# Optimization experiments

Hardware: AMD Instinct MI355X
Metric: run time of the kernel (lower is better)

Reference implementation:

```python
import jax, jax.numpy as jnp
import numpy as np

H = 1024      # hidden_size
I = 4096      # intermediate_size
E = 8         # num_experts
TOP_K = 2
LB_COEF = 0.01


def setup_inputs() -> dict:
    key = jax.random.key(0)
    ks = jax.random.split(key, 8)
    s_h = 1.0 / np.sqrt(H)
    s_i = 1.0 / np.sqrt(I)
    return {
        "x": jax.random.normal(ks[0], (2, 2048, H), dtype=jnp.float32),
        "Wr": jax.random.normal(ks[1], (H, E), dtype=jnp.float32) * s_h,
        "br": jnp.zeros((E,), dtype=jnp.float32),
        "W1": jax.random.normal(ks[2], (E, H, I), dtype=jnp.float32) * s_h,
        "b1": jnp.zeros((E, I), dtype=jnp.float32),
        "W2": jax.random.normal(ks[3], (E, I, H), dtype=jnp.float32) * s_i,
        "b2": jnp.zeros((E, H), dtype=jnp.float32),
    }


def _moe_forward(x, Wr, br, W1, b1, W2, b2):
    B, S, Hd = x.shape
    x_flat = x.reshape(-1, Hd)                      # [T, H]
    T = x_flat.shape[0]

    # ---- Router: softmax probs, top-k, renormalize ----
    logits = x_flat @ Wr + br                       # [T, E]
    probs = jax.nn.softmax(logits, axis=-1)         # [T, E]
    topk_w, topk_idx = jax.lax.top_k(probs, TOP_K)  # [T, K]
    topk_w = topk_w / jnp.sum(topk_w, axis=-1, keepdims=True)

    # ---- Load-balance aux loss (switch-style) ----
    onehot = jax.nn.one_hot(topk_idx, E, dtype=x.dtype)   # [T, K, E]
    frac_tokens = onehot.mean(axis=(0, 1))                 # [E]
    frac_probs = probs.mean(axis=0)                        # [E]
    aux_loss = E * jnp.sum(frac_tokens * frac_probs) * LB_COEF

    # combine_weights[t, e] = routing weight of expert e for token t (0 if unselected)
    combine = jnp.sum(topk_w[..., None] * onehot, axis=1)  # [T, E]

    # ---- Experts: dense per-expert FFN, weighted combine ----
    out = jnp.zeros_like(x_flat)
    for e in range(E):
        h = jax.nn.gelu(x_flat @ W1[e] + b1[e])            # [T, I]
        y = h @ W2[e] + b2[e]                              # [T, H]
        out = out + y * combine[:, e:e + 1]
    return out.reshape(B, S, Hd), aux_loss


def reference(x, Wr, br, W1, b1, W2, b2):
    return _moe_forward(x, Wr, br, W1, b1, W2, b2)
```

## Files before the change

kernel.cpp:

```cpp
#include <hip/hip_runtime.h>
#include <hip/hip_bf16.h>

#define HD 1024
#define ID 4096
#define NE 8
#define NT 4096
#define NSLOT (NT*2)

typedef __attribute__((ext_vector_type(4))) float f32x4;
typedef __attribute__((ext_vector_type(8))) short bf16x8;
typedef __attribute__((ext_vector_type(4))) unsigned int u32x4;
typedef __attribute__((ext_vector_type(2))) unsigned int u32x2;
typedef unsigned short u16;

__device__ __forceinline__ u16 f2b(float f) {
  __hip_bfloat16 h = __float2bfloat16(f);
  return __builtin_bit_cast(unsigned short, h);
}
__device__ __forceinline__ unsigned int pack2(float a, float b) {
  return (unsigned int)f2b(a) | ((unsigned int)f2b(b) << 16);
}
__device__ __forceinline__ void gload16(const void* g, void* l) {
  __builtin_amdgcn_global_load_lds(
      (const __attribute__((address_space(1))) unsigned int*)g,
      (__attribute__((address_space(3))) unsigned int*)l, 16, 0, 0);
}
__device__ __forceinline__ float gelu_tanh(float v) {
  float c = v + 0.044715f * v * v * v;
  return 0.5f * v * (1.0f + tanhf(0.7978845608028654f * c));
}

__global__ void k_convert_x(const float* __restrict__ x, u16* __restrict__ xb) {
  int i = blockIdx.x * 256 + threadIdx.x;
  const f32x4* x4 = (const f32x4*)x;
  f32x4 a = x4[2 * i], b = x4[2 * i + 1];
  u32x4 r;
  r[0] = pack2(a[0], a[1]); r[1] = pack2(a[2], a[3]);
  r[2] = pack2(b[0], b[1]); r[3] = pack2(b[2], b[3]);
  ((u32x4*)xb)[i] = r;
}

__global__ __launch_bounds__(256) void k_transpose_bf16(
    const float* __restrict__ src, u16* __restrict__ dst, int R, int C) {
  __shared__ float tile[64][65];
  int e = blockIdx.z;
  int c0 = blockIdx.x * 64;
  int r0 = blockIdx.y * 64;
  int t = threadIdx.x;
  const float* s = src + (size_t)e * R * C;
#pragma unroll
  for (int i = 0; i < 16; ++i) {
    int r = i * 4 + (t >> 6);
    tile[r][t & 63] = s[(size_t)(r0 + r) * C + c0 + (t & 63)];
  }
  __syncthreads();
  u16* d = dst + (size_t)e * R * C;
#pragma unroll
  for (int i = 0; i < 4; ++i) {
    int c = i * 16 + (t >> 4);
    int rb = (t & 15) * 4;
    u32x2 p;
    p[0] = pack2(tile[rb + 0][c], tile[rb + 1][c]);
    p[1] = pack2(tile[rb + 2][c], tile[rb + 3][c]);
    *(u32x2*)&d[(size_t)(c0 + c) * R + r0 + rb] = p;
  }
}

__global__ __launch_bounds__(256) void k_router(
    const float* __restrict__ x, const float* __restrict__ Wr,
    const float* __restrict__ br, int* __restrict__ cnt,
    int* __restrict__ slotE, int* __restrict__ slotLoc,
    float* __restrict__ slotW, float* __restrict__ probsAll) {
  __shared__ float wrt[NE * HD];
  int t = threadIdx.x;
  for (int i = t; i < NE * HD; i += 256) wrt[(i & 7) * HD + (i >> 3)] = Wr[i];
  __syncthreads();
  int wave = t >> 6, lane = t & 63;
  int token = blockIdx.x * 4 + wave;
  const float* xr = x + (size_t)token * HD;
  float acc[NE] = {0, 0, 0, 0, 0, 0, 0, 0};
#pragma unroll 4
  for (int j = 0; j < 16; ++j) {
    int h = j * 64 + lane;
    float xv = xr[h];
#pragma unroll
    for (int e = 0; e < NE; ++e) acc[e] += xv * wrt[e * HD + h];
  }
#pragma unroll
  for (int d = 1; d < 64; d <<= 1) {
#pragma unroll
    for (int e = 0; e < NE; ++e) acc[e] += __shfl_xor(acc[e], d, 64);
  }
  if (lane == 0) {
    float lg[NE], p[NE];
    float m = -1e30f;
#pragma unroll
    for (int e = 0; e < NE; ++e) { lg[e] = acc[e] + br[e]; m = fmaxf(m, lg[e]); }
    float s = 0.f;
#pragma unroll
    for (int e = 0; e < NE; ++e) { p[e] = expf(lg[e] - m); s += p[e]; }
    float inv = 1.0f / s;
    int i1 = 0, i2 = -1;
    float v1 = -1.f, v2 = -1.f;
#pragma unroll
    for (int e = 0; e < NE; ++e) {
      p[e] *= inv;
      probsAll[token * NE + e] = p[e];
      if (p[e] > v1) { v2 = v1; i2 = i1; v1 = p[e]; i1 = e; }
      else if (p[e] > v2) { v2 = p[e]; i2 = e; }
    }
    float wsum = v1 + v2;
    int l1 = atomicAdd(&cnt[i1], 1);
    int l2 = atomicAdd(&cnt[i2], 1);
    slotE[token * 2] = i1;     slotLoc[token * 2] = l1;     slotW[token * 2] = v1 / wsum;
    slotE[token * 2 + 1] = i2; slotLoc[token * 2 + 1] = l2; slotW[token * 2 + 1] = v2 / wsum;
  }
}

__global__ __launch_bounds__(256) void k_finalize(
    const float* __restrict__ probsAll, const int* __restrict__ cnt,
    int* __restrict__ off, float* __restrict__ out_aux) {
  __shared__ float red[256];
  int t = threadIdx.x;
  float loc[NE] = {0, 0, 0, 0, 0, 0, 0, 0};
  for (int i = t; i < NT; i += 256) {
#pragma unroll
    for (int e = 0; e < NE; ++e) loc[e] += probsAll[i * NE + e];
  }
  __shared__ float psum[NE];
  for (int e = 0; e < NE; ++e) {
    red[t] = loc[e];
    __syncthreads();
    for (int s = 128; s > 0; s >>= 1) {
      if (t < s) red[t] += red[t + s];
      __syncthreads();
    }
    if (t == 0) psum[e] = red[0];
    __syncthreads();
  }
  if (t == 0) {
    int o = 0;
    float a = 0.f;
    for (int e = 0; e < NE; ++e) {
      off[e] = o;
      o += cnt[e];
      a += ((float)cnt[e] / (float)NSLOT) * (psum[e] / (float)NT);
    }
    off[NE] = o;
    out_aux[0] = (float)NE * a * 0.01f;
  }
}

__global__ void k_scatter(const int* __restrict__ slotE, const int* __restrict__ slotLoc,
                          const float* __restrict__ slotW, const int* __restrict__ off,
                          int* __restrict__ rowTok, float* __restrict__ rowW) {
  int i = blockIdx.x * 256 + threadIdx.x;
  int pos = off[slotE[i]] + slotLoc[i];
  if (pos < 0) pos = 0;
  if (pos >= NSLOT) pos = NSLOT - 1;
  rowTok[pos] = i >> 1;
  rowW[pos] = slotW[i];
}

__global__ __launch_bounds__(256, 2) void k_gemm1(
    const u16* __restrict__ xb, const u16* __restrict__ w1t,
    const float* __restrict__ b1, u16* __restrict__ hbuf,
    const int* __restrict__ cnt, const int* __restrict__ off,
    const int* __restrict__ rowTok) {
  int e = blockIdx.z;
  int ce = cnt[e];
  int m0 = blockIdx.y * 128;
  if (m0 >= ce) return;
  int n0 = blockIdx.x * 128;
  int oe = off[e];
  __shared__ u16 As[128 * 32];
  __shared__ u16 Bs[128 * 32];
  __shared__ int rtok[128];
  int t = threadIdx.x;
  if (t < 128) {
    int r = m0 + t;
    if (r >= ce) r = ce - 1;
    int tok = rowTok[oe + r];
    if (tok < 0) tok = 0;
    if (tok >= NT) tok = NT - 1;
    rtok[t] = tok;
  }
  __syncthreads();
  int c0 = t, c1 = t + 256;
  int tokA0 = rtok[c0 >> 2], tokA1 = rtok[c1 >> 2];
  const u16* srcA0 = xb + (size_t)tokA0 * HD + (c0 & 3) * 8;
  const u16* srcA1 = xb + (size_t)tokA1 * HD + (c1 & 3) * 8;
  const u16* bbase = w1t + (size_t)e * ID * HD + (size_t)n0 * HD;
  const u16* srcB0 = bbase + (size_t)(c0 >> 2) * HD + (c0 & 3) * 8;
  const u16* srcB1 = bbase + (size_t)(c1 >> 2) * HD + (c1 & 3) * 8;
  int wave = t >> 6, lane = t & 63;
  int wr = wave >> 1, wc = wave & 1;
  const u16* ap = As + (wr * 64 + (lane & 15)) * 32 + (lane >> 4) * 8;
  const u16* bp = Bs + (wc * 64 + (lane & 15)) * 32 + (lane >> 4) * 8;
  f32x4 acc[4][4] = {};
  for (int kt = 0; kt < HD / 32; ++kt) {
    __syncthreads();
    gload16(srcA0, As + c0 * 8);
    gload16(srcA1, As + c1 * 8);
    gload16(srcB0, Bs + c0 * 8);
    gload16(srcB1, Bs + c1 * 8);
    srcA0 += 32; srcA1 += 32; srcB0 += 32; srcB1 += 32;
    __syncthreads();
    bf16x8 af[4], bfr[4];
#pragma unroll
    for (int m = 0; m < 4; ++m) af[m] = *(const bf16x8*)(ap + m * 16 * 32);
#pragma unroll
    for (int n = 0; n < 4; ++n) bfr[n] = *(const bf16x8*)(bp + n * 16 * 32);
#pragma unroll
    for (int m = 0; m < 4; ++m)
#pragma unroll
      for (int n = 0; n < 4; ++n)
        acc[m][n] = __builtin_amdgcn_mfma_f32_16x16x32_bf16(af[m], bfr[n], acc[m][n], 0, 0, 0);
  }
  const float* b1e = b1 + (size_t)e * ID + n0;
#pragma unroll
  for (int n = 0; n < 4; ++n) {
    int col = wc * 64 + n * 16 + (lane & 15);
    float bias = b1e[col];
#pragma unroll
    for (int m = 0; m < 4; ++m) {
      int rbase = wr * 64 + m * 16 + (lane >> 4) * 4;
#pragma unroll
      for (int r = 0; r < 4; ++r) {
        int grow = m0 + rbase + r;
        if (grow < ce) {
          float v = acc[m][n][r] + bias;
          hbuf[(size_t)(oe + grow) * ID + n0 + col] = f2b(gelu_tanh(v));
        }
      }
    }
  }
}

__global__ __launch_bounds__(256, 2) void k_gemm2(
    const u16* __restrict__ hbuf, const u16* __restrict__ w2t,
    const float* __restrict__ b2, float* __restrict__ ybuf,
    const int* __restrict__ cnt, const int* __restrict__ off,
    const float* __restrict__ rowW) {
  int e = blockIdx.z;
  int ce = cnt[e];
  int m0 = blockIdx.y * 128;
  if (m0 >= ce) return;
  int n0 = blockIdx.x * 128;
  int oe = off[e];
  __shared__ u16 As[128 * 32];
  __shared__ u16 Bs[128 * 32];
  __shared__ float rw[128];
  int t = threadIdx.x;
  if (t < 128) {
    int r = m0 + t;
    rw[t] = (r < ce) ? rowW[oe + r] : 0.0f;
  }
  __syncthreads();
  int c0 = t, c1 = t + 256;
  int rA0 = m0 + (c0 >> 2); if (rA0 >= ce) rA0 = ce - 1;
  int rA1 = m0 + (c1 >> 2); if (rA1 >= ce) rA1 = ce - 1;
  const u16* srcA0 = hbuf + (size_t)(oe + rA0) * ID + (c0 & 3) * 8;
  const u16* srcA1 = hbuf + (size_t)(oe + rA1) * ID + (c1 & 3) * 8;
  const u16* bbase = w2t + (size_t)e * HD * ID + (size_t)n0 * ID;
  const u16* srcB0 = bbase + (size_t)(c0 >> 2) * ID + (c0 & 3) * 8;
  const u16* srcB1 = bbase + (size_t)(c1 >> 2) * ID + (c1 & 3) * 8;
  int wave = t >> 6, lane = t & 63;
  int wr = wave >> 1, wc = wave & 1;
  const u16* ap = As + (wr * 64 + (lane & 15)) * 32 + (lane >> 4) * 8;
  const u16* bp = Bs + (wc * 64 + (lane & 15)) * 32 + (lane >> 4) * 8;
  f32x4 acc[4][4] = {};
  for (int kt = 0; kt < ID / 32; ++kt) {
    __syncthreads();
    gload16(srcA0, As + c0 * 8);
    gload16(srcA1, As + c1 * 8);
    gload16(srcB0, Bs + c0 * 8);
    gload16(srcB1, Bs + c1 * 8);
    srcA0 += 32; srcA1 += 32; srcB0 += 32; srcB1 += 32;
    __syncthreads();
    bf16x8 af[4], bfr[4];
#pragma unroll
    for (int m = 0; m < 4; ++m) af[m] = *(const bf16x8*)(ap + m * 16 * 32);
#pragma unroll
    for (int n = 0; n < 4; ++n) bfr[n] = *(const bf16x8*)(bp + n * 16 * 32);
#pragma unroll
    for (int m = 0; m < 4; ++m)
#pragma unroll
      for (int n = 0; n < 4; ++n)
        acc[m][n] = __builtin_amdgcn_mfma_f32_16x16x32_bf16(af[m], bfr[n], acc[m][n], 0, 0, 0);
  }
  const float* b2e = b2 + (size_t)e * HD + n0;
#pragma unroll
  for (int n = 0; n < 4; ++n) {
    int col = wc * 64 + n * 16 + (lane & 15);
    float bias = b2e[col];
#pragma unroll
    for (int m = 0; m < 4; ++m) {
      int rbase = wr * 64 + m * 16 + (lane >> 4) * 4;
#pragma unroll
      for (int r = 0; r < 4; ++r) {
        int grow = m0 + rbase + r;
        if (grow < ce) {
          float v = (acc[m][n][r] + bias) * rw[rbase + r];
          ybuf[(size_t)(oe + grow) * HD + n0 + col] = v;
        }
      }
    }
  }
}

__global__ void k_combine(const float* __restrict__ ybuf, const int* __restrict__ slotE,
                          const int* __restrict__ slotLoc, const int* __restrict__ off,
                          float* __restrict__ out) {
  int idx = blockIdx.x * 256 + threadIdx.x;
  int token = idx >> 8;
  int c4 = idx & 255;
  int p0 = off[slotE[token * 2]] + slotLoc[token * 2];
  int p1 = off[slotE[token * 2 + 1]] + slotLoc[token * 2 + 1];
  if (p0 < 0) p0 = 0; if (p0 >= NSLOT) p0 = NSLOT - 1;
  if (p1 < 0) p1 = 0; if (p1 >= NSLOT) p1 = NSLOT - 1;
  const f32x4* y4 = (const f32x4*)ybuf;
  f32x4 a = y4[(size_t)p0 * 256 + c4];
  f32x4 b = y4[(size_t)p1 * 256 + c4];
  ((f32x4*)out)[idx] = a + b;
}

extern "C" void kernel_launch(void* const* d_in, const int* in_sizes, int n_in,
                              void* d_out, int out_size, void* d_ws, size_t ws_size,
                              hipStream_t stream) {
  const float* x  = (const float*)d_in[0];
  const float* Wr = (const float*)d_in[1];
  const float* br = (const float*)d_in[2];
  const float* W1 = (const float*)d_in[3];
  const float* b1 = (const float*)d_in[4];
  const float* W2 = (const float*)d_in[5];
  const float* b2 = (const float*)d_in[6];
  float* out = (float*)d_out;

  char* ws = (char*)d_ws;
  size_t o = 0;
  auto alloc = [&](size_t bytes) {
    void* p = ws + o;
    o = (o + bytes + 255) & ~(size_t)255;
    return p;
  };
  u16* xb    = (u16*)alloc((size_t)NT * HD * 2);
  u16* w1t   = (u16*)alloc((size_t)NE * ID * HD * 2);
  u16* w2t   = (u16*)alloc((size_t)NE * ID * HD * 2);
  u16* hbuf  = (u16*)alloc((size_t)NSLOT * ID * 2);
  int* cnt     = (int*)alloc(NE * 4);
  int* off     = (int*)alloc(16 * 4);
  int* slotE   = (int*)alloc(NSLOT * 4);
  int* slotLoc = (int*)alloc(NSLOT * 4);
  float* slotW = (float*)alloc(NSLOT * 4);
  int* rowTok  = (int*)alloc(NSLOT * 4);
  float* rowW  = (float*)alloc(NSLOT * 4);
  float* probsAll = (float*)alloc((size_t)NT * NE * 4);
  float* ybuf = (float*)xb;

  if (ws_size < o) return;

  hipMemsetAsync(cnt, 0, NE * 4, stream);
  k_convert_x<<<(NT * HD / 8) / 256, 256, 0, stream>>>(x, xb);
  k_transpose_bf16<<<dim3(ID / 64, HD / 64, NE), 256, 0, stream>>>(W1, w1t, HD, ID);
  k_transpose_bf16<<<dim3(HD / 64, ID / 64, NE), 256, 0, stream>>>(W2, w2t, ID, HD);
  k_router<<<NT / 4, 256, 0, stream>>>(x, Wr, br, cnt, slotE, slotLoc, slotW, probsAll);
  k_finalize<<<1, 256, 0, stream>>>(probsAll, cnt, off, out + (size_t)NT * HD);
  k_scatter<<<NSLOT / 256, 256, 0, stream>>>(slotE, slotLoc, slotW, off, rowTok, rowW);
  k_gemm1<<<dim3(ID / 128, 32, NE), 256, 0, stream>>>(xb, w1t, b1, hbuf, cnt, off, rowTok);
  k_gemm2<<<dim3(HD / 128, 32, NE), 256, 0, stream>>>(hbuf, w2t, b2, ybuf, cnt, off, rowW);
  k_combine<<<(NT * HD / 4) / 256, 256, 0, stream>>>(ybuf, slotE, slotLoc, off, out);
}
```

Measured before the change: 524.5 us.

## Double-buffer GEMM tiles, remap blocks across XCDs, split-K gemm2 with atomic combine

Both expert GEMMs now use two LDS buffers, so the next K-tile's global-to-LDS loads are issued while MFMAs run on the current tile, and one barrier per iteration is dropped. Launches become 1D with a block-index remap that spreads consecutive workgroups across the XCDs. gemm2 splits K into two halves and atomically adds the routing-weighted result directly into the token-ordered output. That removes the ybuf staging buffer and the separate combine kernel, at the cost of a full output memset and many fp32 atomics with a non-deterministic summation order.

Result: slower. 536.4 us (+2.3%).

```diff
diff --git a/kernel.cpp b/kernel.cpp
--- a/kernel.cpp
+++ b/kernel.cpp
@@ -167,45 +167,57 @@
     const float* __restrict__ b1, u16* __restrict__ hbuf,
     const int* __restrict__ cnt, const int* __restrict__ off,
     const int* __restrict__ rowTok) {
-  int e = blockIdx.z;
+  const int NWG = NE * 32 * 32;
+  int bid = blockIdx.x;
+  int wg = (bid & 7) * (NWG / 8) + (bid >> 3);
+  int e = wg >> 10;
+  int rem = wg & 1023;
+  int m0 = (rem >> 5) * 128;
+  int n0 = (rem & 31) * 128;
   int ce = cnt[e];
-  int m0 = blockIdx.y * 128;
   if (m0 >= ce) return;
-  int n0 = blockIdx.x * 128;
   int oe = off[e];
-  __shared__ u16 As[128 * 32];
-  __shared__ u16 Bs[128 * 32];
+  __shared__ u16 As[2][128 * 32];
+  __shared__ u16 Bs[2][128 * 32];
   __shared__ int rtok[128];
   int t = threadIdx.x;
   if (t < 128) {
     int r = m0 + t;
     if (r >= ce) r = ce - 1;
     int tok = rowTok[oe + r];
-    if (tok < 0) tok = 0;
-    if (tok >= NT) tok = NT - 1;
-    rtok[t] = tok;
+    rtok[t] = (tok < 0) ? 0 : (tok >= NT ? NT - 1 : tok);
   }
   __syncthreads();
   int c0 = t, c1 = t + 256;
-  int tokA0 = rtok[c0 >> 2], tokA1 = rtok[c1 >> 2];
-  const u16* srcA0 = xb + (size_t)tokA0 * HD + (c0 & 3) * 8;
-  const u16* srcA1 = xb + (size_t)tokA1 * HD + (c1 & 3) * 8;
-  const u16* bbase = w1t + (size_t)e * ID * HD + (size_t)n0 * HD;
-  const u16* srcB0 = bbase + (size_t)(c0 >> 2) * HD + (c0 & 3) * 8;
-  const u16* srcB1 = bbase + (size_t)(c1 >> 2) * HD + (c1 & 3) * 8;
+  const u16* srcA0 = xb + (size_t)rtok[c0 >> 2] * HD + (c0 & 3) * 8;
+  const u16* srcA1 = xb + (size_t)rtok[c1 >> 2] * HD + (c1 & 3) * 8;
+  const u16* bb = w1t + (size_t)e * ID * HD + (size_t)n0 * HD;
+  const u16* srcB0 = bb + (size_t)(c0 >> 2) * HD + (c0 & 3) * 8;
+  const u16* srcB1 = bb + (size_t)(c1 >> 2) * HD + (c1 & 3) * 8;
   int wave = t >> 6, lane = t & 63;
   int wr = wave >> 1, wc = wave & 1;
-  const u16* ap = As + (wr * 64 + (lane & 15)) * 32 + (lane >> 4) * 8;
-  const u16* bp = Bs + (wc * 64 + (lane & 15)) * 32 + (lane >> 4) * 8;
+  int aoff = (wr * 64 + (lane & 15)) * 32 + (lane >> 4) * 8;
+  int boff = (wc * 64 + (lane & 15)) * 32 + (lane >> 4) * 8;
   f32x4 acc[4][4] = {};
-  for (int kt = 0; kt < HD / 32; ++kt) {
-    __syncthreads();
-    gload16(srcA0, As + c0 * 8);
-    gload16(srcA1, As + c1 * 8);
-    gload16(srcB0, Bs + c0 * 8);
-    gload16(srcB1, Bs + c1 * 8);
-    srcA0 += 32; srcA1 += 32; srcB0 += 32; srcB1 += 32;
-    __syncthreads();
+  const int NK = HD / 32;
+  gload16(srcA0, &As[0][c0 * 8]);
+  gload16(srcA1, &As[0][c1 * 8]);
+  gload16(srcB0, &Bs[0][c0 * 8]);
+  gload16(srcB1, &Bs[0][c1 * 8]);
+  srcA0 += 32; srcA1 += 32; srcB0 += 32; srcB1 += 32;
+  __syncthreads();
+  int cur = 0;
+  for (int kt = 0;;) {
+    if (kt + 1 < NK) {
+      int nb = cur ^ 1;
+      gload16(srcA0, &As[nb][c0 * 8]);
+      gload16(srcA1, &As[nb][c1 * 8]);
+      gload16(srcB0, &Bs[nb][c0 * 8]);
+      gload16(srcB1, &Bs[nb][c1 * 8]);
+      srcA0 += 32; srcA1 += 32; srcB0 += 32; srcB1 += 32;
+    }
+    const u16* ap = &As[cur][aoff];
+    const u16* bp = &Bs[cur][boff];
     bf16x8 af[4], bfr[4];
 #pragma unroll
     for (int m = 0; m < 4; ++m) af[m] = *(const bf16x8*)(ap + m * 16 * 32);
@@ -216,6 +228,9 @@
 #pragma unroll
       for (int n = 0; n < 4; ++n)
         acc[m][n] = __builtin_amdgcn_mfma_f32_16x16x32_bf16(af[m], bfr[n], acc[m][n], 0, 0, 0);
+    if (++kt == NK) break;
+    __syncthreads();
+    cur ^= 1;
   }
   const float* b1e = b1 + (size_t)e * ID + n0;
 #pragma unroll
@@ -239,45 +254,66 @@
 
 __global__ __launch_bounds__(256, 2) void k_gemm2(
     const u16* __restrict__ hbuf, const u16* __restrict__ w2t,
-    const float* __restrict__ b2, float* __restrict__ ybuf,
+    const float* __restrict__ b2, float* __restrict__ out,
     const int* __restrict__ cnt, const int* __restrict__ off,
-    const float* __restrict__ rowW) {
-  int e = blockIdx.z;
+    const int* __restrict__ rowTok, const float* __restrict__ rowW) {
+  const int NWG = NE * 32 * 2 * 8;
+  int bid = blockIdx.x;
+  int wg = (bid & 7) * (NWG / 8) + (bid >> 3);
+  int e = wg >> 9;
+  int rem = wg & 511;
+  int m0 = (rem >> 4) * 128;
+  int ks = (rem >> 3) & 1;
+  int n0 = (rem & 7) * 128;
   int ce = cnt[e];
-  int m0 = blockIdx.y * 128;
   if (m0 >= ce) return;
-  int n0 = blockIdx.x * 128;
   int oe = off[e];
-  __shared__ u16 As[128 * 32];
-  __shared__ u16 Bs[128 * 32];
+  int k0 = ks * (ID / 2);
+  __shared__ u16 As[2][128 * 32];
+  __shared__ u16 Bs[2][128 * 32];
+  __shared__ int rtok[128];
   __shared__ float rw[128];
   int t = threadIdx.x;
   if (t < 128) {
     int r = m0 + t;
+    int rc = (r < ce) ? r : ce - 1;
+    int tok = rowTok[oe + rc];
+    rtok[t] = (tok < 0) ? 0 : (tok >= NT ? NT - 1 : tok);
     rw[t] = (r < ce) ? rowW[oe + r] : 0.0f;
   }
   __syncthreads();
   int c0 = t, c1 = t + 256;
   int rA0 = m0 + (c0 >> 2); if (rA0 >= ce) rA0 = ce - 1;
   int rA1 = m0 + (c1 >> 2); if (rA1 >= ce) rA1 = ce - 1;
-  const u16* srcA0 = hbuf + (size_t)(oe + rA0) * ID + (c0 & 3) * 8;
-  const u16* srcA1 = hbuf + (size_t)(oe + rA1) * ID + (c1 & 3) * 8;
-  const u16* bbase = w2t + (size_t)e * HD * ID + (size_t)n0 * ID;
-  const u16* srcB0 = bbase + (size_t)(c0 >> 2) * ID + (c0 & 3) * 8;
-  const u16* srcB1 = bbase + (size_t)(c1 >> 2) * ID + (c1 & 3) * 8;
+  const u16* srcA0 = hbuf + (size_t)(oe + rA0) * ID + k0 + (c0 & 3) * 8;
+  const u16* srcA1 = hbuf + (size_t)(oe + rA1) * ID + k0 + (c1 & 3) * 8;
+  const u16* bb = w2t + (size_t)e * HD * ID + (size_t)n0 * ID + k0;
+  const u16* srcB0 = bb + (size_t)(c0 >> 2) * ID + (c0 & 3) * 8;
+  const u16* srcB1 = bb + (size_t)(c1 >> 2) * ID + (c1 & 3) * 8;
   int wave = t >> 6, lane = t & 63;
   int wr = wave >> 1, wc = wave & 1;
-  const u16* ap = As + (wr * 64 + (lane & 15)) * 32 + (lane >> 4) * 8;
-  const u16* bp = Bs + (wc * 64 + (lane & 15)) * 32 + (lane >> 4) * 8;
+  int aoff = (wr * 64 + (lane & 15)) * 32 + (lane >> 4) * 8;
+  int boff = (wc * 64 + (lane & 15)) * 32 + (lane >> 4) * 8;
   f32x4 acc[4][4] = {};
-  for (int kt = 0; kt < ID / 32; ++kt) {
-    __syncthreads();
-    gload16(srcA0, As + c0 * 8);
-    gload16(srcA1, As + c1 * 8);
-    gload16(srcB0, Bs + c0 * 8);
-    gload16(srcB1, Bs + c1 * 8);
-    srcA0 += 32; srcA1 += 32; srcB0 += 32; srcB1 += 32;
-    __syncthreads();
+  const int NK = (ID / 2) / 32;
+  gload16(srcA0, &As[0][c0 * 8]);
+  gload16(srcA1, &As[0][c1 * 8]);
+  gload16(srcB0, &Bs[0][c0 * 8]);
+  gload16(srcB1, &Bs[0][c1 * 8]);
+  srcA0 += 32; srcA1 += 32; srcB0 += 32; srcB1 += 32;
+  __syncthreads();
+  int cur = 0;
+  for (int kt = 0;;) {
+    if (kt + 1 < NK) {
+      int nb = cur ^ 1;
+      gload16(srcA0, &As[nb][c0 * 8]);
+      gload16(srcA1, &As[nb][c1 * 8]);
+      gload16(srcB0, &Bs[nb][c0 * 8]);
+      gload16(srcB1, &Bs[nb][c1 * 8]);
+      srcA0 += 32; srcA1 += 32; srcB0 += 32; srcB1 += 32;
+    }
+    const u16* ap = &As[cur][aoff];
+    const u16* bp = &Bs[cur][boff];
     bf16x8 af[4], bfr[4];
 #pragma unroll
     for (int m = 0; m < 4; ++m) af[m] = *(const bf16x8*)(ap + m * 16 * 32);
@@ -288,12 +324,15 @@
 #pragma unroll
       for (int n = 0; n < 4; ++n)
         acc[m][n] = __builtin_amdgcn_mfma_f32_16x16x32_bf16(af[m], bfr[n], acc[m][n], 0, 0, 0);
+    if (++kt == NK) break;
+    __syncthreads();
+    cur ^= 1;
   }
   const float* b2e = b2 + (size_t)e * HD + n0;
 #pragma unroll
   for (int n = 0; n < 4; ++n) {
     int col = wc * 64 + n * 16 + (lane & 15);
-    float bias = b2e[col];
+    float bias = (ks == 0) ? b2e[col] : 0.0f;
 #pragma unroll
     for (int m = 0; m < 4; ++m) {
       int rbase = wr * 64 + m * 16 + (lane >> 4) * 4;
@@ -302,27 +341,11 @@
         int grow = m0 + rbase + r;
         if (grow < ce) {
           float v = (acc[m][n][r] + bias) * rw[rbase + r];
-          ybuf[(size_t)(oe + grow) * HD + n0 + col] = v;
+          atomicAdd(&out[(size_t)rtok[rbase + r] * HD + n0 + col], v);
         }
       }
     }
   }
-}
-
-__global__ void k_combine(const float* __restrict__ ybuf, const int* __restrict__ slotE,
-                          const int* __restrict__ slotLoc, const int* __restrict__ off,
-                          float* __restrict__ out) {
-  int idx = blockIdx.x * 256 + threadIdx.x;
-  int token = idx >> 8;
-  int c4 = idx & 255;
-  int p0 = off[slotE[token * 2]] + slotLoc[token * 2];
-  int p1 = off[slotE[token * 2 + 1]] + slotLoc[token * 2 + 1];
-  if (p0 < 0) p0 = 0; if (p0 >= NSLOT) p0 = NSLOT - 1;
-  if (p1 < 0) p1 = 0; if (p1 >= NSLOT) p1 = NSLOT - 1;
-  const f32x4* y4 = (const f32x4*)ybuf;
-  f32x4 a = y4[(size_t)p0 * 256 + c4];
-  f32x4 b = y4[(size_t)p1 * 256 + c4];
-  ((f32x4*)out)[idx] = a + b;
 }
 
 extern "C" void kernel_launch(void* const* d_in, const int* in_sizes, int n_in,
@@ -356,18 +379,17 @@
   int* rowTok  = (int*)alloc(NSLOT * 4);
   float* rowW  = (float*)alloc(NSLOT * 4);
   float* probsAll = (float*)alloc((size_t)NT * NE * 4);
-  float* ybuf = (float*)xb;
 
   if (ws_size < o) return;
 
   hipMemsetAsync(cnt, 0, NE * 4, stream);
+  hipMemsetAsync(out, 0, (size_t)out_size * 4, stream);
   k_convert_x<<<(NT * HD / 8) / 256, 256, 0, stream>>>(x, xb);
   k_transpose_bf16<<<dim3(ID / 64, HD / 64, NE), 256, 0, stream>>>(W1, w1t, HD, ID);
   k_transpose_bf16<<<dim3(HD / 64, ID / 64, NE), 256, 0, stream>>>(W2, w2t, ID, HD);
   k_router<<<NT / 4, 256, 0, stream>>>(x, Wr, br, cnt, slotE, slotLoc, slotW, probsAll);
   k_finalize<<<1, 256, 0, stream>>>(probsAll, cnt, off, out + (size_t)NT * HD);
   k_scatter<<<NSLOT / 256, 256, 0, stream>>>(slotE, slotLoc, slotW, off, rowTok, rowW);
-  k_gemm1<<<dim3(ID / 128, 32, NE), 256, 0, stream>>>(xb, w1t, b1, hbuf, cnt, off, rowTok);
-  k_gemm2<<<dim3(HD / 128, 32, NE), 256, 0, stream>>>(hbuf, w2t, b2, ybuf, cnt, off, rowW);
-  k_combine<<<(NT * HD / 4) / 256, 256, 0, stream>>>(ybuf, slotE, slotLoc, off, out);
-}
+  k_gemm1<<<NE * 32 * 32, 256, 0, stream>>>(xb, w1t, b1, hbuf, cnt, off, rowTok);
+  k_gemm2<<<NE * 32 * 2 * 8, 256, 0, stream>>>(hbuf, w2t, b2, out, cnt, off, rowTok, rowW);
+}
```
